# Optimization experiments

Hardware: AMD Instinct MI355X
Metric: run time of the kernel (lower is better)

## Reference

```python
import jax, jax.numpy as jnp
import numpy as np

ALPHA = 0.7
NUM_HEADS = 12
NUM_KV_HEADS = 6
HEAD_DIM = 64
ROPE_BASE = 10000.0


def ternary_quantize(w):
    thr = ALPHA * jnp.mean(jnp.abs(w))
    return jnp.sign(w) * (jnp.abs(w) >= thr).astype(w.dtype)


def bitlinear(x, w):
    # forward: F.linear(x, ternary(w)) * mean(|w|)
    scale = jnp.mean(jnp.abs(w))
    qw = ternary_quantize(w)
    return (x @ qw.T) * scale


def rope_tables(seq_len, dim, dtype):
    inv_freq = 1.0 / (ROPE_BASE ** (jnp.arange(0, dim, 2, dtype=jnp.float32) / dim))
    t = jnp.arange(seq_len, dtype=jnp.float32)
    freqs = jnp.outer(t, inv_freq)            # [S, dim/2]
    emb = jnp.concatenate([freqs, freqs], -1)  # [S, dim]
    return jnp.cos(emb).astype(dtype), jnp.sin(emb).astype(dtype)


def rotate_half(x):
    x1, x2 = jnp.split(x, 2, axis=-1)
    return jnp.concatenate([-x2, x1], axis=-1)


def setup_inputs() -> dict:
    key = jax.random.key(0)
    ks = jax.random.split(key, 5)
    B, S, H = 2, 2048, 768
    return {
        "hidden_states": jax.random.normal(ks[0], (B, S, H), jnp.float32),
        "Wq": jax.random.normal(ks[1], (768, 768), jnp.float32) * 0.02,
        "Wk": jax.random.normal(ks[2], (384, 768), jnp.float32) * 0.02,
        "Wv": jax.random.normal(ks[3], (384, 768), jnp.float32) * 0.02,
        "Wo": jax.random.normal(ks[4], (768, 768), jnp.float32) * 0.02,
    }


def reference(hidden_states, Wq, Wk, Wv, Wo):
    B, S, H = hidden_states.shape
    nh, nkv, hd = NUM_HEADS, NUM_KV_HEADS, HEAD_DIM
    groups = nh // nkv

    q = bitlinear(hidden_states, Wq).reshape(B, S, nh, hd).transpose(0, 2, 1, 3)
    k = bitlinear(hidden_states, Wk).reshape(B, S, nkv, hd).transpose(0, 2, 1, 3)
    v = bitlinear(hidden_states, Wv).reshape(B, S, nkv, hd).transpose(0, 2, 1, 3)

    cos, sin = rope_tables(S, hd, hidden_states.dtype)  # [S, hd]
    cos = cos[None, None]  # [1,1,S,hd]
    sin = sin[None, None]
    q = q * cos + rotate_half(q) * sin
    k = k * cos + rotate_half(k) * sin

    # GQA: expand kv heads to full head count
    k = jnp.repeat(k, groups, axis=1)  # [B, nh, S, hd]
    v = jnp.repeat(v, groups, axis=1)

    scale = 1.0 / jnp.sqrt(jnp.asarray(hd, hidden_states.dtype))
    scores = jnp.einsum("bhsd,bhtd->bhst", q, k) * scale
    attn = jax.nn.softmax(scores, axis=-1)
    out = jnp.einsum("bhst,bhtd->bhsd", attn, v)
    out = out.transpose(0, 2, 1, 3).reshape(B, S, H)
    return bitlinear(out, Wo)
```

## Files before the change

### kernel.cpp

```cpp
#include <hip/hip_runtime.h>
#include <cmath>

typedef unsigned short u16;
typedef unsigned int u32;
typedef __bf16 bf16x2 __attribute__((ext_vector_type(2)));
typedef __bf16 bf16x8 __attribute__((ext_vector_type(8)));
typedef float f32x2 __attribute__((ext_vector_type(2)));
typedef float f32x16 __attribute__((ext_vector_type(16)));

#define NQ (768*768)
#define NK (384*768)

__device__ __forceinline__ u16 f2bf(float f) {
  u32 u = __float_as_uint(f);
  u32 r = (u + 0x7FFFu + ((u >> 16) & 1u)) >> 16;
  return (u16)r;
}
__device__ __forceinline__ u32 packbf(float a, float b) {
#if __has_builtin(__builtin_amdgcn_cvt_pk_bf16_f32)
  bf16x2 v = __builtin_amdgcn_cvt_pk_bf16_f32(a, b);
  u32 r; __builtin_memcpy(&r, &v, 4); return r;
#else
  return (u32)f2bf(a) | ((u32)f2bf(b) << 16);
#endif
}
__device__ __forceinline__ float fexp2(float x) {
#if __has_builtin(__builtin_amdgcn_exp2f)
  return __builtin_amdgcn_exp2f(x);
#else
  return exp2f(x);
#endif
}
__device__ __forceinline__ bf16x8 ldfrag(const u16* p) { bf16x8 v; __builtin_memcpy(&v, p, 16); return v; }
__device__ __forceinline__ f32x16 mfma32_(bf16x8 a, bf16x8 b, f32x16 c) {
  return __builtin_amdgcn_mfma_f32_32x32x16_bf16(a, b, c, 0, 0, 0);
}
__device__ __forceinline__ void gload_lds16(const u16* g, u16* l) {
  __builtin_amdgcn_global_load_lds((const __attribute__((address_space(1))) void*)g,
                                   (__attribute__((address_space(3))) void*)l, 16, 0, 0);
}
__device__ __forceinline__ int xcd_swz768(int lin) { return (lin & 7) * 96 + (lin >> 3); }

__device__ __forceinline__ int fidx(int r, int k) {
  return (r >> 5) * 24576 + (k >> 4) * 512 + ((r & 31) + 32 * ((k >> 3) & 1)) * 8 + (k & 7);
}
__device__ __forceinline__ int kidx(int b6kvh, int s, int d) {
  return b6kvh * 131072 + (s >> 5) * 2048 + (d >> 4) * 512 +
         ((s & 31) + 32 * ((d >> 3) & 1)) * 8 + (d & 7);
}
__device__ __forceinline__ int qidx(int b, int s, int h, int d) {
  return ((b * 64 + (s >> 5)) * 12 + h) * 2048 + (d >> 4) * 512 +
         ((s & 31) + 32 * ((d >> 3) & 1)) * 8 + (d & 7);
}
__device__ __forceinline__ int vidx(int b6kvh, int d, int p) {
  return b6kvh * 131072 + (p >> 6) * 4096 + (d >> 5) * 2048 + ((p >> 4) & 3) * 512 +
         ((d & 31) + 32 * ((p >> 3) & 1)) * 8 + (p & 7);
}

__global__ __launch_bounds__(256) void abssum_kernel(const float* __restrict__ wq, const float* __restrict__ wk,
                                                     const float* __restrict__ wv, const float* __restrict__ wo,
                                                     float* __restrict__ sums, float2* __restrict__ rt) {
  int which = blockIdx.y;
  const float* w = (which == 0) ? wq : (which == 1) ? wk : (which == 2) ? wv : wo;
  int n4 = ((which == 0 || which == 3) ? NQ : NK) >> 2;
  const float4* w4 = (const float4*)w;
  float s = 0.f;
  for (int i = blockIdx.x * blockDim.x + threadIdx.x; i < n4; i += gridDim.x * blockDim.x) {
    float4 v = w4[i];
    s += fabsf(v.x) + fabsf(v.y) + fabsf(v.z) + fabsf(v.w);
  }
  for (int off = 32; off; off >>= 1) s += __shfl_down(s, off);
  __shared__ float ls[4];
  if ((threadIdx.x & 63) == 0) ls[threadIdx.x >> 6] = s;
  __syncthreads();
  if (threadIdx.x == 0) atomicAdd(&sums[which], ls[0] + ls[1] + ls[2] + ls[3]);
  int gid = (blockIdx.y * 64 + blockIdx.x) * 256 + threadIdx.x;
  int sr = gid >> 5, cc = gid & 31;
  float f = exp2f((float)cc * -0.41524101186092029f);
  float sn, cs; sincosf((float)sr * f, &sn, &cs);
  rt[gid] = make_float2(cs, sn);
}

__global__ __launch_bounds__(256) void prep_kernel(const float* __restrict__ wq, const float* __restrict__ wk,
                                                   const float* __restrict__ wv, const float* __restrict__ wo,
                                                   const float* __restrict__ sums, const float* __restrict__ x,
                                                   u16* __restrict__ qw, u16* __restrict__ woq,
                                                   u16* __restrict__ xb) {
  int i = blockIdx.x * blockDim.x + threadIdx.x;
  if (i < 221184) {
    int n = i / 96, k8 = i - n * 96;
    const float* src; float th; u16* dst; int nd;
    if (n < 768)       { src = wq + n * 768;          th = 0.7f * sums[0] * (1.f / NQ); dst = qw;  nd = n; }
    else if (n < 1152) { src = wk + (n - 768) * 768;  th = 0.7f * sums[1] * (1.f / NK); dst = qw;  nd = n; }
    else if (n < 1536) { src = wv + (n - 1152) * 768; th = 0.7f * sums[2] * (1.f / NK); dst = qw;  nd = n; }
    else               { src = wo + (n - 1536) * 768; th = 0.7f * sums[3] * (1.f / NQ); dst = woq; nd = n - 1536; }
    const float4* sp = (const float4*)(src + k8 * 8);
    float4 v0 = sp[0], v1 = sp[1];
    float e[8] = {v0.x, v0.y, v0.z, v0.w, v1.x, v1.y, v1.z, v1.w};
    u16 o[8];
#pragma unroll
    for (int j = 0; j < 8; j++)
      o[j] = f2bf((fabsf(e[j]) >= th) ? ((e[j] > 0.f) ? 1.f : -1.f) : 0.f);
    __builtin_memcpy(dst + fidx(nd, k8 * 8), o, 16);
  } else {
    int j = i - 221184;
    int m = j / 96, k8 = j - m * 96;
    const float4* xp = (const float4*)(x + m * 768 + k8 * 8);
    float4 v0 = xp[0], v1 = xp[1];
    u16 o[8] = { f2bf(v0.x), f2bf(v0.y), f2bf(v0.z), f2bf(v0.w),
                 f2bf(v1.x), f2bf(v1.y), f2bf(v1.z), f2bf(v1.w) };
    __builtin_memcpy(xb + fidx(m, k8 * 8), o, 16);
  }
}

__global__ __launch_bounds__(256, 3) void gemm_qkv_kernel(const u16* __restrict__ xb, const u16* __restrict__ qw,
                                                          const float* __restrict__ sums,
                                                          const float2* __restrict__ rt,
                                                          u16* __restrict__ qb, u16* __restrict__ kb,
                                                          u16* __restrict__ vT) {
  __shared__ u16 sm[24 * 512];
  int v = xcd_swz768(blockIdx.x);
  int tm = v / 12, tn = v - tm * 12;
  int t = threadIdx.x, lane = t & 63, w = t >> 6, c = lane & 31, g2 = lane >> 5;
  int wm = w & 1, wn = w >> 1;
  int wn8 = wn * 8;

  f32x16 acc[2]; acc[0] = (f32x16)0.f; acc[1] = (f32x16)0.f;

  for (int s = 0; s < 12; ++s) {
#pragma unroll
    for (int i = 0; i < 6; i++) {
      int ch = w * 6 + i;
      const u16* src = (ch < 8)
        ? xb + (tm * 2 + (ch >> 2)) * 24576 + (s * 4 + (ch & 3)) * 512 + lane * 8
        : qw + (tn * 4 + (ch >> 2) - 2) * 24576 + (s * 4 + (ch & 3)) * 512 + lane * 8;
      gload_lds16(src, sm + ch * 512);
    }
    __syncthreads();
#pragma unroll
    for (int kc = 0; kc < 4; kc++) {
      bf16x8 a  = ldfrag(sm + (wm * 4 + kc) * 512 + lane * 8);
      bf16x8 b0 = ldfrag(sm + (8 + wn8 + kc) * 512 + lane * 8);
      bf16x8 b1 = ldfrag(sm + (12 + wn8 + kc) * 512 + lane * 8);
      acc[0] = mfma32_(a, b0, acc[0]);
      acc[1] = mfma32_(a, b1, acc[1]);
    }
    __syncthreads();
  }

  float sq = sums[0] * (1.f / NQ) * 0.180336880111120f;
  float sk = sums[1] * (1.f / NK);
  float sv = sums[2] * (1.f / NK);
  int mb = tm * 64 + wm * 32 + 4 * g2;
  if (tn < 9) {
    float sc = (tn < 6) ? sq : sk;
    int head = (tn < 6) ? (tn * 2 + wn) : ((tn - 6) * 2 + wn);
    const float2* rp = rt + c;
#pragma unroll
    for (int r = 0; r < 16; r++) {
      int m = mb + (r & 3) + 8 * (r >> 2);
      int bb = m >> 11, s = m & 2047;
      float2 cs2 = rp[s << 5];
      float x1 = acc[0][r] * sc, x2 = acc[1][r] * sc;
      u16 y1 = f2bf(x1 * cs2.x - x2 * cs2.y);
      u16 y2 = f2bf(x2 * cs2.x + x1 * cs2.y);
      if (tn < 6) {
        qb[qidx(bb, s, head, c)]      = y1;
        qb[qidx(bb, s, head, c + 32)] = y2;
      } else {
        kb[kidx(bb * 6 + head, s, c)]      = y1;
        kb[kidx(bb * 6 + head, s, c + 32)] = y2;
      }
    }
  } else {
    int kvh = (tn - 9) * 2 + wn;
#pragma unroll
    for (int nb = 0; nb < 2; nb++)
#pragma unroll
      for (int r = 0; r < 16; r++) {
        int m = mb + (r & 3) + 8 * (r >> 2);
        int bb = m >> 11, s = m & 2047;
        int sp = (s & ~12) | ((s & 4) << 1) | ((s & 8) >> 1);
        vT[vidx(bb * 6 + kvh, nb * 32 + c, sp)] = f2bf(acc[nb][r] * sv);
      }
  }
}

__device__ __forceinline__ void attn_step_pair(const bf16x8 (&kf)[4], const bf16x8 (&vf)[2][2],
                                               const bf16x8 (&qf0)[4], const bf16x8 (&qf1)[4],
                                               f32x16 (&O0)[2], f32x16 (&O1)[2],
                                               float& lsum0, float& lsum1) {
  f32x16 S = (f32x16)0.f;
  __builtin_amdgcn_s_setprio(1);
#pragma unroll
  for (int ks = 0; ks < 4; ks++) S = mfma32_(kf[ks], qf0[ks], S);
  __builtin_amdgcn_s_setprio(0);
#pragma unroll
  for (int r = 0; r < 16; r++) S[r] = fexp2(S[r]);
  {
    f32x2 a0 = {S[0], S[1]},  a1 = {S[2], S[3]},  a2 = {S[4], S[5]},  a3 = {S[6], S[7]};
    f32x2 a4 = {S[8], S[9]},  a5 = {S[10], S[11]}, a6 = {S[12], S[13]}, a7 = {S[14], S[15]};
    f32x2 b0 = a0 + a1, b1 = a2 + a3, b2 = a4 + a5, b3 = a6 + a7;
    f32x2 c0 = b0 + b1, c1 = b2 + b3;
    f32x2 d = c0 + c1;
    lsum0 += d.x + d.y;
  }
  u32 P[8];
#pragma unroll
  for (int j = 0; j < 8; j++) P[j] = packbf(S[2 * j], S[2 * j + 1]);
  bf16x8 PA0, PA1;
  __builtin_memcpy(&PA0, &P[0], 16);
  __builtin_memcpy(&PA1, &P[4], 16);
  f32x16 S1 = (f32x16)0.f;
  __builtin_amdgcn_s_setprio(1);
  O0[0] = mfma32_(PA0, vf[0][0], O0[0]);
  S1 = mfma32_(kf[0], qf1[0], S1);
  O0[1] = mfma32_(PA0, vf[1][0], O0[1]);
  S1 = mfma32_(kf[1], qf1[1], S1);
  O0[0] = mfma32_(PA1, vf[0][1], O0[0]);
  S1 = mfma32_(kf[2], qf1[2], S1);
  O0[1] = mfma32_(PA1, vf[1][1], O0[1]);
  S1 = mfma32_(kf[3], qf1[3], S1);
  __builtin_amdgcn_s_setprio(0);
#pragma unroll
  for (int r = 0; r < 16; r++) S1[r] = fexp2(S1[r]);
  {
    f32x2 a0 = {S1[0], S1[1]},  a1 = {S1[2], S1[3]},  a2 = {S1[4], S1[5]},  a3 = {S1[6], S1[7]};
    f32x2 a4 = {S1[8], S1[9]},  a5 = {S1[10], S1[11]}, a6 = {S1[12], S1[13]}, a7 = {S1[14], S1[15]};
    f32x2 b0 = a0 + a1, b1 = a2 + a3, b2 = a4 + a5, b3 = a6 + a7;
    f32x2 c0 = b0 + b1, c1 = b2 + b3;
    f32x2 d = c0 + c1;
    lsum1 += d.x + d.y;
  }
#pragma unroll
  for (int j = 0; j < 8; j++) P[j] = packbf(S1[2 * j], S1[2 * j + 1]);
  bf16x8 PB0, PB1;
  __builtin_memcpy(&PB0, &P[0], 16);
  __builtin_memcpy(&PB1, &P[4], 16);
  __builtin_amdgcn_s_setprio(1);
  O1[0] = mfma32_(PB0, vf[0][0], O1[0]);
  O1[1] = mfma32_(PB0, vf[1][0], O1[1]);
  O1[0] = mfma32_(PB1, vf[0][1], O1[0]);
  O1[1] = mfma32_(PB1, vf[1][1], O1[1]);
  __builtin_amdgcn_s_setprio(0);
}

__global__ __launch_bounds__(256, 3) void attn_kernel(const u16* __restrict__ qb, const u16* __restrict__ kb,
                                                      const u16* __restrict__ vT, u16* __restrict__ ab) {
  __shared__ float Obuf[4][32][66];
  __shared__ float Lbuf[4][32];
  int v = xcd_swz768(blockIdx.x);
  int bk = v >> 6, y = v & 63;
  int b = bk / 6, kvh = bk % 6;
  int qp = y & 31, h2 = y >> 5;
  int h = kvh * 2 + h2;
  int t = threadIdx.x, lane = t & 63, w = t >> 6, c = lane & 31, g2 = lane >> 5;

  const u16* q0 = qb + ((b * 64 + qp * 2) * 12 + h) * 2048 + lane * 8;
  const u16* q1 = q0 + 12 * 2048;
  bf16x8 qf0[4], qf1[4];
#pragma unroll
  for (int ks = 0; ks < 4; ks++) { qf0[ks] = ldfrag(q0 + ks * 512); qf1[ks] = ldfrag(q1 + ks * 512); }

  f32x16 fz = (f32x16)0.f;
  f32x16 O0[2] = {fz, fz}, O1[2] = {fz, fz};
  float lsum0 = 0.f, lsum1 = 0.f;

  const u16* Kb = kb + bk * 131072;
  const u16* Vb = vT + bk * 131072;

  for (int it = 0; it < 16; ++it) {
    int g = w * 16 + it;
    const u16* kt = Kb + g * 2048 + lane * 8;
    const u16* vt = Vb + (g >> 1) * 4096 + (g & 1) * 1024 + lane * 8;
    bf16x8 kf[4], vf[2][2];
#pragma unroll
    for (int ks = 0; ks < 4; ks++) kf[ks] = ldfrag(kt + ks * 512);
#pragma unroll
    for (int dn = 0; dn < 2; dn++)
#pragma unroll
      for (int ksv = 0; ksv < 2; ksv++)
        vf[dn][ksv] = ldfrag(vt + dn * 2048 + ksv * 512);
    attn_step_pair(kf, vf, qf0, qf1, O0, O1, lsum0, lsum1);
  }

  float lt0 = lsum0 + __shfl_xor(lsum0, 32);
  float lt1 = lsum1 + __shfl_xor(lsum1, 32);

#pragma unroll
  for (int qi = 0; qi < 2; qi++) {
    if (qi) __syncthreads();
    if (g2 == 0) Lbuf[w][c] = qi ? lt1 : lt0;
    const f32x16* Ow = qi ? O1 : O0;
#pragma unroll
    for (int dn = 0; dn < 2; dn++)
#pragma unroll
      for (int r = 0; r < 16; r++)
        Obuf[w][(r & 3) + 8 * (r >> 2) + 4 * g2][dn * 32 + c] = Ow[dn][r];
    __syncthreads();
    int qq = t >> 3, col8 = (t & 7) * 8;
    float l = Lbuf[0][qq] + Lbuf[1][qq] + Lbuf[2][qq] + Lbuf[3][qq];
    float inv = 1.f / l;
    u16 o[8];
#pragma unroll
    for (int j = 0; j < 8; j++)
      o[j] = f2bf((Obuf[0][qq][col8 + j] + Obuf[1][qq][col8 + j] +
                   Obuf[2][qq][col8 + j] + Obuf[3][qq][col8 + j]) * inv);
    int mg = b * 64 + qp * 2 + qi;
    u16* dst = ab + mg * 24576 + ((h * 64 + col8) >> 4) * 512 + ((col8 >> 3) & 1) * 256 + qq * 8;
    __builtin_memcpy(dst, o, 16);
  }
}

__global__ __launch_bounds__(256, 3) void gemm_out_kernel(const u16* __restrict__ ab, const u16* __restrict__ woq,
                                                          const float* __restrict__ sums, float* __restrict__ out) {
  __shared__ u16 sm[32 * 512];
  int v = xcd_swz768(blockIdx.x);
  int tm = v / 12, tn = v - tm * 12;
  int t = threadIdx.x, lane = t & 63, w = t >> 6, c = lane & 31, g2 = lane >> 5;
  int wm = w & 1, wn = w >> 1;

  f32x16 acc = (f32x16)0.f;

  for (int s = 0; s < 6; ++s) {
#pragma unroll
    for (int i = 0; i < 8; i++) {
      int ch = w * 8 + i;
      const u16* src = (ch < 16)
        ? ab + (tm * 2 + (ch >> 3)) * 24576 + (s * 8 + (ch & 7)) * 512 + lane * 8
        : woq + (tn * 2 + (ch >> 3) - 2) * 24576 + (s * 8 + (ch & 7)) * 512 + lane * 8;
      gload_lds16(src, sm + ch * 512);
    }
    __syncthreads();
#pragma unroll
    for (int kc = 0; kc < 8; kc++) {
      bf16x8 a = ldfrag(sm + (wm * 8 + kc) * 512 + lane * 8);
      bf16x8 b = ldfrag(sm + (16 + wn * 8 + kc) * 512 + lane * 8);
      acc = mfma32_(a, b, acc);
    }
    __syncthreads();
  }

  float so = sums[3] * (1.f / NQ);
  int mb = tm * 64 + wm * 32 + 4 * g2;
#pragma unroll
  for (int r = 0; r < 16; r++) {
    int m = mb + (r & 3) + 8 * (r >> 2);
    out[m * 768 + tn * 64 + wn * 32 + c] = acc[r] * so;
  }
}

extern "C" void kernel_launch(void* const* d_in, const int* in_sizes, int n_in,
                              void* d_out, int out_size, void* d_ws, size_t ws_size,
                              hipStream_t stream) {
  const float* x  = (const float*)d_in[0];
  const float* wq = (const float*)d_in[1];
  const float* wk = (const float*)d_in[2];
  const float* wv = (const float*)d_in[3];
  const float* wo = (const float*)d_in[4];
  float* out = (float*)d_out;
  char* ws = (char*)d_ws;

  float* sums = (float*)ws;
  u16* qw  = (u16*)(ws + 256);
  u16* woq = (u16*)(ws + 2359552);
  u16* xb  = (u16*)(ws + 3539200);
  u16* qb  = (u16*)(ws + 9830656);
  u16* kb  = (u16*)(ws + 16122112);
  u16* vT  = (u16*)(ws + 19267840);
  u16* ab  = (u16*)(ws + 22413568);
  float2* rt = (float2*)(ws + 28705024);

  hipMemsetAsync(sums, 0, 16, stream);
  dim3 blk(256);
  abssum_kernel<<<dim3(64, 4), blk, 0, stream>>>(wq, wk, wv, wo, sums, rt);
  prep_kernel<<<dim3(2400), blk, 0, stream>>>(wq, wk, wv, wo, sums, x, qw, woq, xb);
  gemm_qkv_kernel<<<dim3(768), blk, 0, stream>>>(xb, qw, sums, rt, qb, kb, vT);
  attn_kernel<<<dim3(768), blk, 0, stream>>>(qb, kb, vT, ab);
  gemm_out_kernel<<<dim3(768), blk, 0, stream>>>(ab, woq, sums, out);
}
```

Before: 146.4 us.

## Software-pipeline attention loop with K double-buffering and cross-iteration MFMA interleave

Restructures the attention inner loop so K fragments for the next tile are prefetched into a double buffer, and the next tile's QK^T for query block 0 is interleaved with the current PV MFMAs for query block 1. The loop is fully unrolled, and the V loads for the next tile are issued after the last use of the current V. This aims to hide global-load latency and the exp/pack VALU work behind MFMA execution. In exchange it raises register pressure (two K buffers plus a live S0 across iterations), which could hurt occupancy under launch_bounds(256,3) or cause spills.

```diff
diff --git a/kernel.cpp b/kernel.cpp
--- a/kernel.cpp
+++ b/kernel.cpp
@@ -186,62 +186,51 @@
   }
 }
 
-__device__ __forceinline__ void attn_step_pair(const bf16x8 (&kf)[4], const bf16x8 (&vf)[2][2],
-                                               const bf16x8 (&qf0)[4], const bf16x8 (&qf1)[4],
-                                               f32x16 (&O0)[2], f32x16 (&O1)[2],
-                                               float& lsum0, float& lsum1) {
-  f32x16 S = (f32x16)0.f;
+__device__ __forceinline__ void qk_cluster(const bf16x8 (&kf)[4], const bf16x8 (&qf)[4], f32x16& S) {
   __builtin_amdgcn_s_setprio(1);
 #pragma unroll
-  for (int ks = 0; ks < 4; ks++) S = mfma32_(kf[ks], qf0[ks], S);
+  for (int ks = 0; ks < 4; ks++) S = mfma32_(kf[ks], qf[ks], S);
   __builtin_amdgcn_s_setprio(0);
+}
+__device__ __forceinline__ float exp_sum(f32x16& S) {
 #pragma unroll
   for (int r = 0; r < 16; r++) S[r] = fexp2(S[r]);
-  {
-    f32x2 a0 = {S[0], S[1]},  a1 = {S[2], S[3]},  a2 = {S[4], S[5]},  a3 = {S[6], S[7]};
-    f32x2 a4 = {S[8], S[9]},  a5 = {S[10], S[11]}, a6 = {S[12], S[13]}, a7 = {S[14], S[15]};
-    f32x2 b0 = a0 + a1, b1 = a2 + a3, b2 = a4 + a5, b3 = a6 + a7;
-    f32x2 c0 = b0 + b1, c1 = b2 + b3;
-    f32x2 d = c0 + c1;
-    lsum0 += d.x + d.y;
-  }
+  f32x2 a0 = {S[0], S[1]},  a1 = {S[2], S[3]},  a2 = {S[4], S[5]},  a3 = {S[6], S[7]};
+  f32x2 a4 = {S[8], S[9]},  a5 = {S[10], S[11]}, a6 = {S[12], S[13]}, a7 = {S[14], S[15]};
+  f32x2 b0 = a0 + a1, b1 = a2 + a3, b2 = a4 + a5, b3 = a6 + a7;
+  f32x2 c0 = b0 + b1, c1 = b2 + b3;
+  f32x2 d = c0 + c1;
+  return d.x + d.y;
+}
+__device__ __forceinline__ void pack_p(const f32x16& S, bf16x8& P0, bf16x8& P1) {
   u32 P[8];
 #pragma unroll
   for (int j = 0; j < 8; j++) P[j] = packbf(S[2 * j], S[2 * j + 1]);
-  bf16x8 PA0, PA1;
-  __builtin_memcpy(&PA0, &P[0], 16);
-  __builtin_memcpy(&PA1, &P[4], 16);
-  f32x16 S1 = (f32x16)0.f;
+  __builtin_memcpy(&P0, &P[0], 16);
+  __builtin_memcpy(&P1, &P[4], 16);
+}
+__device__ __forceinline__ void pv_qk_cluster(const bf16x8& PA0, const bf16x8& PA1,
+                                              const bf16x8 (&vf)[2][2], f32x16 (&O)[2],
+                                              const bf16x8 (&kf)[4], const bf16x8 (&qf)[4],
+                                              f32x16& S) {
   __builtin_amdgcn_s_setprio(1);
-  O0[0] = mfma32_(PA0, vf[0][0], O0[0]);
-  S1 = mfma32_(kf[0], qf1[0], S1);
-  O0[1] = mfma32_(PA0, vf[1][0], O0[1]);
-  S1 = mfma32_(kf[1], qf1[1], S1);
-  O0[0] = mfma32_(PA1, vf[0][1], O0[0]);
-  S1 = mfma32_(kf[2], qf1[2], S1);
-  O0[1] = mfma32_(PA1, vf[1][1], O0[1]);
-  S1 = mfma32_(kf[3], qf1[3], S1);
+  O[0] = mfma32_(PA0, vf[0][0], O[0]);
+  S = mfma32_(kf[0], qf[0], S);
+  O[1] = mfma32_(PA0, vf[1][0], O[1]);
+  S = mfma32_(kf[1], qf[1], S);
+  O[0] = mfma32_(PA1, vf[0][1], O[0]);
+  S = mfma32_(kf[2], qf[2], S);
+  O[1] = mfma32_(PA1, vf[1][1], O[1]);
+  S = mfma32_(kf[3], qf[3], S);
   __builtin_amdgcn_s_setprio(0);
-#pragma unroll
-  for (int r = 0; r < 16; r++) S1[r] = fexp2(S1[r]);
-  {
-    f32x2 a0 = {S1[0], S1[1]},  a1 = {S1[2], S1[3]},  a2 = {S1[4], S1[5]},  a3 = {S1[6], S1[7]};
-    f32x2 a4 = {S1[8], S1[9]},  a5 = {S1[10], S1[11]}, a6 = {S1[12], S1[13]}, a7 = {S1[14], S1[15]};
-    f32x2 b0 = a0 + a1, b1 = a2 + a3, b2 = a4 + a5, b3 = a6 + a7;
-    f32x2 c0 = b0 + b1, c1 = b2 + b3;
-    f32x2 d = c0 + c1;
-    lsum1 += d.x + d.y;
-  }
-#pragma unroll
-  for (int j = 0; j < 8; j++) P[j] = packbf(S1[2 * j], S1[2 * j + 1]);
-  bf16x8 PB0, PB1;
-  __builtin_memcpy(&PB0, &P[0], 16);
-  __builtin_memcpy(&PB1, &P[4], 16);
+}
+__device__ __forceinline__ void pv_cluster(const bf16x8& P0, const bf16x8& P1,
+                                           const bf16x8 (&vf)[2][2], f32x16 (&O)[2]) {
   __builtin_amdgcn_s_setprio(1);
-  O1[0] = mfma32_(PB0, vf[0][0], O1[0]);
-  O1[1] = mfma32_(PB0, vf[1][0], O1[1]);
-  O1[0] = mfma32_(PB1, vf[0][1], O1[0]);
-  O1[1] = mfma32_(PB1, vf[1][1], O1[1]);
+  O[0] = mfma32_(P0, vf[0][0], O[0]);
+  O[1] = mfma32_(P0, vf[1][0], O[1]);
+  O[0] = mfma32_(P1, vf[0][1], O[0]);
+  O[1] = mfma32_(P1, vf[1][1], O[1]);
   __builtin_amdgcn_s_setprio(0);
 }
 
@@ -269,19 +258,49 @@
   const u16* Kb = kb + bk * 131072;
   const u16* Vb = vT + bk * 131072;
 
-  for (int it = 0; it < 16; ++it) {
-    int g = w * 16 + it;
-    const u16* kt = Kb + g * 2048 + lane * 8;
-    const u16* vt = Vb + (g >> 1) * 4096 + (g & 1) * 1024 + lane * 8;
-    bf16x8 kf[4], vf[2][2];
-#pragma unroll
-    for (int ks = 0; ks < 4; ks++) kf[ks] = ldfrag(kt + ks * 512);
+  bf16x8 kf[2][4], vf[2][2];
+  int g0 = w * 16;
+  {
+    const u16* kt = Kb + g0 * 2048 + lane * 8;
+#pragma unroll
+    for (int ks = 0; ks < 4; ks++) kf[0][ks] = ldfrag(kt + ks * 512);
+    const u16* vt = Vb + (g0 >> 1) * 4096 + (g0 & 1) * 1024 + lane * 8;
 #pragma unroll
     for (int dn = 0; dn < 2; dn++)
 #pragma unroll
       for (int ksv = 0; ksv < 2; ksv++)
         vf[dn][ksv] = ldfrag(vt + dn * 2048 + ksv * 512);
-    attn_step_pair(kf, vf, qf0, qf1, O0, O1, lsum0, lsum1);
+  }
+  f32x16 S0 = fz;
+  qk_cluster(kf[0], qf0, S0);
+
+#pragma unroll
+  for (int it = 0; it < 16; ++it) {
+    const int cur = it & 1, nxt = cur ^ 1;
+    if (it < 15) {
+      const u16* kt = Kb + (g0 + it + 1) * 2048 + lane * 8;
+#pragma unroll
+      for (int ks = 0; ks < 4; ks++) kf[nxt][ks] = ldfrag(kt + ks * 512);
+    }
+    lsum0 += exp_sum(S0);
+    bf16x8 PA0, PA1; pack_p(S0, PA0, PA1);
+    f32x16 S1 = fz;
+    pv_qk_cluster(PA0, PA1, vf, O0, kf[cur], qf1, S1);
+    lsum1 += exp_sum(S1);
+    bf16x8 PB0, PB1; pack_p(S1, PB0, PB1);
+    if (it < 15) {
+      S0 = fz;
+      pv_qk_cluster(PB0, PB1, vf, O1, kf[nxt], qf0, S0);
+      int gn = g0 + it + 1;
+      const u16* vt = Vb + (gn >> 1) * 4096 + (gn & 1) * 1024 + lane * 8;
+#pragma unroll
+      for (int dn = 0; dn < 2; dn++)
+#pragma unroll
+        for (int ksv = 0; ksv < 2; ksv++)
+          vf[dn][ksv] = ldfrag(vt + dn * 2048 + ksv * 512);
+    } else {
+      pv_cluster(PB0, PB1, vf, O1);
+    }
   }
 
   float lt0 = lsum0 + __shfl_xor(lsum0, 32);
```

New measurement: 214.2 us. 46.3% more time.
